# Optimization experiments

Measured on AMD Instinct MI355X. Metric: run time of the kernel, lower is better.

Reference implementation:

```python
import jax, jax.numpy as jnp
import numpy as np

EMB_DIM = 768
NUM_HEADS = 12
HEAD_DIM = EMB_DIM // NUM_HEADS
B, S = 8, 1024


def setup_inputs() -> dict:
    key = jax.random.key(0)
    ks = jax.random.split(key, 8)
    q = jax.random.normal(ks[0], (B, S, EMB_DIM), dtype=jnp.float32)
    k = jax.random.normal(ks[1], (B, S, EMB_DIM), dtype=jnp.float32)
    v = jax.random.normal(ks[2], (B, S, EMB_DIM), dtype=jnp.float32)
    # Per-head projection weights, torch nn.Linear layout [out_dim, in_dim]
    xav = float(np.sqrt(6.0 / (HEAD_DIM + HEAD_DIM)))
    Wq = jax.random.uniform(ks[3], (NUM_HEADS, HEAD_DIM, HEAD_DIM), jnp.float32, -xav, xav)
    Wk = jax.random.uniform(ks[4], (NUM_HEADS, HEAD_DIM, HEAD_DIM), jnp.float32, -xav, xav)
    Wv = jax.random.uniform(ks[5], (NUM_HEADS, HEAD_DIM, HEAD_DIM), jnp.float32, -xav, xav)
    # Output projection (torch Linear default init scale not critical for correctness baseline)
    bound = float(1.0 / np.sqrt(EMB_DIM))
    Wo = jax.random.uniform(ks[6], (EMB_DIM, EMB_DIM), jnp.float32, -bound, bound)
    bo = jax.random.uniform(ks[7], (EMB_DIM,), jnp.float32, -bound, bound)
    return {"q": q, "k": k, "v": v, "Wq": Wq, "Wk": Wk, "Wv": Wv, "Wo": Wo, "bo": bo}


def reference(q, k, v, Wq, Wk, Wv, Wo, bo):
    b, s, _ = q.shape
    # split heads: [B, S, E] -> [B, H, S, d]
    def split(x):
        return x.reshape(b, s, NUM_HEADS, HEAD_DIM).transpose(0, 2, 1, 3)
    qh, kh, vh = split(q), split(k), split(v)
    # per-head linear (torch: y = x @ W^T), vectorized over heads
    Q = jnp.einsum('bhsd,hod->bhso', qh, Wq)
    K = jnp.einsum('bhsd,hod->bhso', kh, Wk)
    V = jnp.einsum('bhsd,hod->bhso', vh, Wv)
    scale = 1.0 / jnp.sqrt(jnp.float32(HEAD_DIM))
    scores = jnp.einsum('bhqd,bhkd->bhqk', Q, K) * scale  # [B,H,S,S]
    weights = jax.nn.softmax(scores, axis=-1)
    attn = jnp.einsum('bhqk,bhkd->bhqd', weights, V)
    # merge heads: [B,H,S,d] -> [B,S,E]
    attn = attn.transpose(0, 2, 1, 3).reshape(b, s, EMB_DIM)
    return attn @ Wo.T + bo
```

## Files before the change

kernel.cpp:

```cpp
#include <hip/hip_runtime.h>
#include <hip/hip_bf16.h>

#define BB 8
#define SS 1024
#define EE 768
#define HH 12
#define DD 64
#define NT (BB*SS)

typedef __attribute__((ext_vector_type(8))) short bf16x8;
typedef __attribute__((ext_vector_type(4))) float f32x4;

__device__ __forceinline__ ushort f2bf(float f) {
  union { float f; unsigned u; } x; x.f = f;
  unsigned r = x.u + 0x7fffu + ((x.u >> 16) & 1u);
  return (ushort)(r >> 16);
}

__device__ __forceinline__ unsigned cvtpk(float a, float b) {
  unsigned r;
  asm("v_cvt_pk_bf16_f32 %0, %1, %2" : "=v"(r) : "v"(a), "v"(b));
  return r;
}

__device__ __forceinline__ void gl2lds(const void* g, void* l) {
  __builtin_amdgcn_global_load_lds(
      (const __attribute__((address_space(1))) unsigned int*)g,
      (__attribute__((address_space(3))) unsigned int*)l, 16, 0, 0);
}

__global__ void cvt_weights(const float* __restrict__ Wq, const float* __restrict__ Wk,
                            const float* __restrict__ Wv, const float* __restrict__ Wo,
                            ushort* __restrict__ Wqb, ushort* __restrict__ Wkb,
                            ushort* __restrict__ Wvb, ushort* __restrict__ Wob) {
  int i = blockIdx.x * blockDim.x + threadIdx.x;
  const int NW = HH*DD*DD;
  if (i < NW) { Wqb[i] = f2bf(Wq[i]); Wkb[i] = f2bf(Wk[i]); Wvb[i] = f2bf(Wv[i]); }
  if (i < EE*EE) Wob[i] = f2bf(Wo[i]);
}

__global__ __launch_bounds__(256) void proj_qkv(
    const float* __restrict__ q, const float* __restrict__ k, const float* __restrict__ v,
    const ushort* __restrict__ Wqb, const ushort* __restrict__ Wkb, const ushort* __restrict__ Wvb,
    ushort* __restrict__ Qb, ushort* __restrict__ Kb, ushort* __restrict__ Vt) {
  int bid = blockIdx.x;
  int m  = bid / (BB*HH*(SS/64));
  int r  = bid % (BB*HH*(SS/64));
  int bh = r / (SS/64);
  int st = r % (SS/64);

  const float*  x = (m==0 ? q : (m==1 ? k : v)) + ((size_t)((bh/HH)*SS + st*64))*EE + (bh%HH)*DD;
  const ushort* W = (m==0 ? Wqb : (m==1 ? Wkb : Wvb)) + (bh%HH)*DD*DD;

  int tid = threadIdx.x;
  int w = tid >> 6, l = tid & 63;
  int lr = l & 15, lg = l >> 4;

  bf16x8 a[2];
  const float* xr = x + (size_t)(w*16 + lr)*EE;
#pragma unroll
  for (int ks = 0; ks < 2; ++ks) {
    f32x4 t0 = *(const f32x4*)(xr + ks*32 + lg*8);
    f32x4 t1 = *(const f32x4*)(xr + ks*32 + lg*8 + 4);
    bf16x8 av;
#pragma unroll
    for (int j = 0; j < 4; ++j) { av[j] = (short)f2bf(t0[j]); av[4+j] = (short)f2bf(t1[j]); }
    a[ks] = av;
  }

  f32x4 acc[4] = {};
  if (m == 2) {
#pragma unroll
    for (int f = 0; f < 4; ++f) {
      bf16x8 b0 = *(const bf16x8*)(W + (f*16 + lr)*DD + lg*8);
      bf16x8 b1 = *(const bf16x8*)(W + (f*16 + lr)*DD + 32 + lg*8);
      acc[f] = __builtin_amdgcn_mfma_f32_16x16x32_bf16(a[0], b0, acc[f], 0, 0, 0);
      acc[f] = __builtin_amdgcn_mfma_f32_16x16x32_bf16(a[1], b1, acc[f], 0, 0, 0);
    }
    int posb = st*64 + 32*(w>>1) + 8*lg + 4*(w&1);
#pragma unroll
    for (int f = 0; f < 4; ++f) {
      ushort2 p0, p1;
      *(unsigned*)&p0 = cvtpk(acc[f][0], acc[f][1]);
      *(unsigned*)&p1 = cvtpk(acc[f][2], acc[f][3]);
      ushort4 pk; pk.x = p0.x; pk.y = p0.y; pk.z = p1.x; pk.w = p1.y;
      *(ushort4*)(Vt + ((size_t)bh*DD + f*16 + lr)*SS + posb) = pk;
    }
  } else {
#pragma unroll
    for (int f = 0; f < 4; ++f) {
      bf16x8 b0 = *(const bf16x8*)(W + (f*16 + lr)*DD + lg*8);
      bf16x8 b1 = *(const bf16x8*)(W + (f*16 + lr)*DD + 32 + lg*8);
      acc[f] = __builtin_amdgcn_mfma_f32_16x16x32_bf16(b0, a[0], acc[f], 0, 0, 0);
      acc[f] = __builtin_amdgcn_mfma_f32_16x16x32_bf16(b1, a[1], acc[f], 0, 0, 0);
    }
    float qscale = (m == 0) ? 0.18033688011112042f : 1.0f;
    ushort* dst = (m == 0 ? Qb : Kb) + ((size_t)bh*SS + st*64 + w*16 + lr)*DD;
#pragma unroll
    for (int f = 0; f < 4; ++f) {
      ushort2 p0, p1;
      *(unsigned*)&p0 = cvtpk(acc[f][0]*qscale, acc[f][1]*qscale);
      *(unsigned*)&p1 = cvtpk(acc[f][2]*qscale, acc[f][3]*qscale);
      ushort4 pk; pk.x = p0.x; pk.y = p0.y; pk.z = p1.x; pk.w = p1.y;
      *(ushort4*)(dst + f*16 + lg*4) = pk;
    }
  }
}

__global__ __launch_bounds__(256) void attn_fwd(
    const ushort* __restrict__ Qb, const ushort* __restrict__ Kb,
    const ushort* __restrict__ Vt, ushort* __restrict__ attn) {
  __shared__ uint4 ldsq[3072];
  char* ldsb = (char*)ldsq;

  int bid = blockIdx.x;
  int bh = bid % (BB*HH);
  int qt = bid / (BB*HH);
  int b = bh / HH, h = bh % HH;
  int tid = threadIdx.x, w = tid >> 6, l = tid & 63;
  int lr = l & 15, lg = l >> 4;

  const ushort* Qp0 = Qb + ((size_t)bh*SS + qt*128 + w*32 + lr)*DD;
  bf16x8 bq[2][2];
  bq[0][0] = *(const bf16x8*)(Qp0 + lg*8);
  bq[0][1] = *(const bf16x8*)(Qp0 + 32 + lg*8);
  bq[1][0] = *(const bf16x8*)(Qp0 + 16*DD + lg*8);
  bq[1][1] = *(const bf16x8*)(Qp0 + 16*DD + 32 + lg*8);

  const ushort* Kbh = Kb + (size_t)bh*SS*DD;
  const ushort* Vbh = Vt + (size_t)bh*DD*SS;

  const short ONE = (short)0x3F80;
  bf16x8 ones = {ONE, ONE, ONE, ONE, ONE, ONE, ONE, ONE};

  f32x4 lsum[2] = {};
  f32x4 o[2][4] = {};

#define STAGE(bufidx, kt) do {                                                   \
    char* LK_ = ldsb + (bufidx)*16384;                                           \
    const ushort* ksrc = Kbh + ((size_t)((kt)*64 + w*16 + lr))*DD + lg*8;        \
    const ushort* vsrc = Vbh + ((size_t)(w*16 + lr))*SS + (kt)*64 + lg*8;        \
    gl2lds(ksrc,      LK_ + tid*16);                                             \
    gl2lds(ksrc + 32, LK_ + 4096 + tid*16);                                      \
    gl2lds(vsrc,      LK_ + 8192 + tid*16);                                      \
    gl2lds(vsrc + 32, LK_ + 12288 + tid*16);                                     \
  } while (0)

  STAGE(0, 0);
  STAGE(1, 1);
  int bi = 0;
  for (int kt = 0; kt < 16; ++kt) {
    const char* LK_ = ldsb + bi*16384;
    const char* LV_ = LK_ + 8192;

    if (kt < 15) { asm volatile("s_waitcnt vmcnt(4)" ::: "memory"); }
    else         { asm volatile("s_waitcnt vmcnt(0)" ::: "memory"); }
    __builtin_amdgcn_s_barrier();
    __builtin_amdgcn_sched_barrier(0);

    int pi = bi + 2; if (pi >= 3) pi -= 3;
    if (kt < 14) STAGE(pi, kt + 2);

    f32x4 st0[4] = {}, st1[4] = {};
    __builtin_amdgcn_s_setprio(1);
#pragma unroll
    for (int f = 0; f < 4; ++f) {
      bf16x8 k0 = *(const bf16x8*)(LK_ + f*1024 + l*16);
      bf16x8 k1 = *(const bf16x8*)(LK_ + 4096 + f*1024 + l*16);
      st0[f] = __builtin_amdgcn_mfma_f32_16x16x32_bf16(k0, bq[0][0], st0[f], 0, 0, 0);
      st0[f] = __builtin_amdgcn_mfma_f32_16x16x32_bf16(k1, bq[0][1], st0[f], 0, 0, 0);
      st1[f] = __builtin_amdgcn_mfma_f32_16x16x32_bf16(k0, bq[1][0], st1[f], 0, 0, 0);
      st1[f] = __builtin_amdgcn_mfma_f32_16x16x32_bf16(k1, bq[1][1], st1[f], 0, 0, 0);
    }
    __builtin_amdgcn_s_setprio(0);

    union { bf16x8 v; unsigned u[4]; } pba[2], pbb[2];
#pragma unroll
    for (int s = 0; s < 2; ++s) {
      f32x4* st = (s == 0) ? st0 : st1;
#pragma unroll
      for (int f = 0; f < 4; ++f) {
#pragma unroll
        for (int j = 0; j < 4; ++j) st[f][j] = __builtin_amdgcn_exp2f(st[f][j]);
      }
      pba[s].u[0] = cvtpk(st[0][0], st[0][1]); pba[s].u[1] = cvtpk(st[0][2], st[0][3]);
      pba[s].u[2] = cvtpk(st[1][0], st[1][1]); pba[s].u[3] = cvtpk(st[1][2], st[1][3]);
      pbb[s].u[0] = cvtpk(st[2][0], st[2][1]); pbb[s].u[1] = cvtpk(st[2][2], st[2][3]);
      pbb[s].u[2] = cvtpk(st[3][0], st[3][1]); pbb[s].u[3] = cvtpk(st[3][2], st[3][3]);
    }

    __builtin_amdgcn_s_setprio(1);
#pragma unroll
    for (int f = 0; f < 4; ++f) {
      bf16x8 va = *(const bf16x8*)(LV_ + f*1024 + l*16);
      bf16x8 vc = *(const bf16x8*)(LV_ + 4096 + f*1024 + l*16);
      o[0][f] = __builtin_amdgcn_mfma_f32_16x16x32_bf16(va, pba[0].v, o[0][f], 0, 0, 0);
      o[0][f] = __builtin_amdgcn_mfma_f32_16x16x32_bf16(vc, pbb[0].v, o[0][f], 0, 0, 0);
      o[1][f] = __builtin_amdgcn_mfma_f32_16x16x32_bf16(va, pba[1].v, o[1][f], 0, 0, 0);
      o[1][f] = __builtin_amdgcn_mfma_f32_16x16x32_bf16(vc, pbb[1].v, o[1][f], 0, 0, 0);
    }
    lsum[0] = __builtin_amdgcn_mfma_f32_16x16x32_bf16(ones, pba[0].v, lsum[0], 0, 0, 0);
    lsum[0] = __builtin_amdgcn_mfma_f32_16x16x32_bf16(ones, pbb[0].v, lsum[0], 0, 0, 0);
    lsum[1] = __builtin_amdgcn_mfma_f32_16x16x32_bf16(ones, pba[1].v, lsum[1], 0, 0, 0);
    lsum[1] = __builtin_amdgcn_mfma_f32_16x16x32_bf16(ones, pbb[1].v, lsum[1], 0, 0, 0);
    __builtin_amdgcn_s_setprio(0);

    bi = (bi == 2) ? 0 : bi + 1;
  }
#undef STAGE

#pragma unroll
  for (int s = 0; s < 2; ++s) {
    float inv = 1.0f / lsum[s][0];
    ushort* orow = attn + ((size_t)(b*SS + qt*128 + w*32 + s*16 + lr))*EE + h*DD;
#pragma unroll
    for (int f = 0; f < 4; ++f) {
      ushort4 pkd;
      pkd.x = f2bf(o[s][f][0] * inv);
      pkd.y = f2bf(o[s][f][1] * inv);
      pkd.z = f2bf(o[s][f][2] * inv);
      pkd.w = f2bf(o[s][f][3] * inv);
      *(ushort4*)(orow + f*16 + lg*4) = pkd;
    }
  }
}

__global__ __launch_bounds__(256) void out_proj(
    const ushort* __restrict__ attn, const ushort* __restrict__ Wob,
    const float* __restrict__ bo, float* __restrict__ out) {
  __shared__ uint4 ldsq[3072];
  char* ldsb = (char*)ldsq;

  int bid = blockIdx.x;
  int mt = bid & 127;
  int nt = bid >> 7;
  int tid = threadIdx.x, w = tid >> 6, l = tid & 63;
  int lr = l & 15, lg = l >> 4;

  int rS = tid >> 3;
  int cSw = (((tid & 7) * 16) ^ ((rS & 7) << 4)) >> 1;

  const ushort* Abase = attn + ((size_t)mt*64)*EE;
  const ushort* Bbase = Wob + ((size_t)nt*128)*EE;

#define OSTAGE(bufidx, kt) do {                                                  \
    char* LA_ = ldsb + (bufidx)*24576;                                           \
    char* LB_ = LA_ + 8192;                                                      \
    const ushort* asrc = Abase + (kt)*64 + cSw;                                  \
    const ushort* bsrc = Bbase + (kt)*64 + cSw;                                  \
    gl2lds(asrc + (size_t)rS*EE,        LA_ + tid*16);                           \
    gl2lds(asrc + (size_t)(rS+32)*EE,   LA_ + 4096 + tid*16);                    \
    gl2lds(bsrc + (size_t)rS*EE,        LB_ + tid*16);                           \
    gl2lds(bsrc + (size_t)(rS+32)*EE,   LB_ + 4096 + tid*16);                    \
    gl2lds(bsrc + (size_t)(rS+64)*EE,   LB_ + 8192 + tid*16);                    \
    gl2lds(bsrc + (size_t)(rS+96)*EE,   LB_ + 12288 + tid*16);                   \
  } while (0)

  f32x4 acc[4][2] = {};

#define OCOMPUTE(bufidx) do {                                                    \
    const char* LA_ = ldsb + (bufidx)*24576;                                     \
    const char* LB_ = LA_ + 8192;                                                \
    bf16x8 af[4][2], bf[2][2];                                                   \
    _Pragma("unroll")                                                            \
    for (int f = 0; f < 4; ++f) {                                                \
      int row = f*16 + lr; int sw = (row & 7) << 4;                              \
      af[f][0] = *(const bf16x8*)(LA_ + row*128 + ((lg*16) ^ sw));               \
      af[f][1] = *(const bf16x8*)(LA_ + row*128 + ((64 + lg*16) ^ sw));          \
    }                                                                            \
    _Pragma("unroll")                                                            \
    for (int g = 0; g < 2; ++g) {                                                \
      int row = w*32 + g*16 + lr; int sw = (row & 7) << 4;                       \
      bf[g][0] = *(const bf16x8*)(LB_ + row*128 + ((lg*16) ^ sw));               \
      bf[g][1] = *(const bf16x8*)(LB_ + row*128 + ((64 + lg*16) ^ sw));          \
    }                                                                            \
    _Pragma("unroll")                                                            \
    for (int f = 0; f < 4; ++f) {                                                \
      _Pragma("unroll")                                                          \
      for (int g = 0; g < 2; ++g) {                                              \
        acc[f][g] = __builtin_amdgcn_mfma_f32_16x16x32_bf16(af[f][0], bf[g][0], acc[f][g], 0, 0, 0); \
        acc[f][g] = __builtin_amdgcn_mfma_f32_16x16x32_bf16(af[f][1], bf[g][1], acc[f][g], 0, 0, 0); \
      }                                                                          \
    }                                                                            \
  } while (0)

  OSTAGE(0, 0);
  __syncthreads();
  for (int kt = 0; kt < EE/64; ++kt) {
    if (kt < EE/64 - 1) OSTAGE((kt + 1) & 1, kt + 1);
    OCOMPUTE(kt & 1);
    __syncthreads();
  }
#undef OSTAGE
#undef OCOMPUTE

#pragma unroll
  for (int g = 0; g < 2; ++g) {
    int col = nt*128 + w*32 + g*16 + lr;
    float bias = bo[col];
#pragma unroll
    for (int f = 0; f < 4; ++f) {
#pragma unroll
      for (int j = 0; j < 4; ++j) {
        int row = mt*64 + f*16 + lg*4 + j;
        out[(size_t)row*EE + col] = acc[f][g][j] + bias;
      }
    }
  }
}

extern "C" void kernel_launch(void* const* d_in, const int* in_sizes, int n_in,
                              void* d_out, int out_size, void* d_ws, size_t ws_size,
                              hipStream_t stream) {
  (void)in_sizes; (void)n_in; (void)out_size; (void)ws_size;
  const float* q  = (const float*)d_in[0];
  const float* k  = (const float*)d_in[1];
  const float* v  = (const float*)d_in[2];
  const float* Wq = (const float*)d_in[3];
  const float* Wk = (const float*)d_in[4];
  const float* Wv = (const float*)d_in[5];
  const float* Wo = (const float*)d_in[6];
  const float* bo = (const float*)d_in[7];
  float* out = (float*)d_out;

  char* ws = (char*)d_ws;
  const size_t SZ = (size_t)BB*HH*SS*DD*2;
  ushort* Qb   = (ushort*)(ws);
  ushort* Kb   = (ushort*)(ws + SZ);
  ushort* Vt   = (ushort*)(ws + 2*SZ);
  ushort* attn = (ushort*)(ws + 3*SZ);
  ushort* Wqb  = (ushort*)(ws + 4*SZ);
  ushort* Wkb  = (ushort*)(ws + 4*SZ +   98304);
  ushort* Wvb  = (ushort*)(ws + 4*SZ + 2*98304);
  ushort* Wob  = (ushort*)(ws + 4*SZ + 3*98304);

  cvt_weights<<<(EE*EE + 255)/256, 256, 0, stream>>>(Wq, Wk, Wv, Wo, Wqb, Wkb, Wvb, Wob);
  proj_qkv<<<3*BB*HH*(SS/64), 256, 0, stream>>>(q, k, v, Wqb, Wkb, Wvb, Qb, Kb, Vt);
  attn_fwd<<<BB*HH*(SS/128), 256, 0, stream>>>(Qb, Kb, Vt, attn);
  out_proj<<<(NT/64)*(EE/128), 256, 0, stream>>>(attn, Wob, bo, out);
}
```

Measured before the change: 90.21 us.

## Convert QKV weights in-kernel and relax out_proj barriers with partial vmcnt waits

proj_qkv now reads the fp32 per-head weights directly and converts them with packed bf16 instructions, so cvt_weights only handles Wo and the separate bf16 copies of Wq/Wk/Wv go away. The input activation conversion also switches from scalar rounding to v_cvt_pk_bf16_f32. In out_proj, the full __syncthreads after each stage is replaced by raw s_barrier plus an explicit s_waitcnt vmcnt(6), so the next stage's global-to-LDS loads can stay in flight during compute. The cost is that each projection block re-reads fp32 weights, doubling weight traffic, and the code now depends on the vmcnt count matching the number of loads issued per stage.

```diff
diff --git a/kernel.cpp b/kernel.cpp
--- a/kernel.cpp
+++ b/kernel.cpp
@@ -29,19 +29,16 @@
       (__attribute__((address_space(3))) unsigned int*)l, 16, 0, 0);
 }
 
-__global__ void cvt_weights(const float* __restrict__ Wq, const float* __restrict__ Wk,
-                            const float* __restrict__ Wv, const float* __restrict__ Wo,
-                            ushort* __restrict__ Wqb, ushort* __restrict__ Wkb,
-                            ushort* __restrict__ Wvb, ushort* __restrict__ Wob) {
+#define MFMA16(A, B, C) __builtin_amdgcn_mfma_f32_16x16x32_bf16((A), (B), (C), 0, 0, 0)
+
+__global__ void cvt_weights(const float* __restrict__ Wo, ushort* __restrict__ Wob) {
   int i = blockIdx.x * blockDim.x + threadIdx.x;
-  const int NW = HH*DD*DD;
-  if (i < NW) { Wqb[i] = f2bf(Wq[i]); Wkb[i] = f2bf(Wk[i]); Wvb[i] = f2bf(Wv[i]); }
   if (i < EE*EE) Wob[i] = f2bf(Wo[i]);
 }
 
 __global__ __launch_bounds__(256) void proj_qkv(
     const float* __restrict__ q, const float* __restrict__ k, const float* __restrict__ v,
-    const ushort* __restrict__ Wqb, const ushort* __restrict__ Wkb, const ushort* __restrict__ Wvb,
+    const float* __restrict__ Wq, const float* __restrict__ Wk, const float* __restrict__ Wv,
     ushort* __restrict__ Qb, ushort* __restrict__ Kb, ushort* __restrict__ Vt) {
   int bid = blockIdx.x;
   int m  = bid / (BB*HH*(SS/64));
@@ -49,33 +46,37 @@
   int bh = r / (SS/64);
   int st = r % (SS/64);
 
-  const float*  x = (m==0 ? q : (m==1 ? k : v)) + ((size_t)((bh/HH)*SS + st*64))*EE + (bh%HH)*DD;
-  const ushort* W = (m==0 ? Wqb : (m==1 ? Wkb : Wvb)) + (bh%HH)*DD*DD;
+  const float* x = (m==0 ? q : (m==1 ? k : v)) + ((size_t)((bh/HH)*SS + st*64))*EE + (bh%HH)*DD;
+  const float* W = (m==0 ? Wq : (m==1 ? Wk : Wv)) + (bh%HH)*DD*DD;
 
   int tid = threadIdx.x;
   int w = tid >> 6, l = tid & 63;
   int lr = l & 15, lg = l >> 4;
 
-  bf16x8 a[2];
+  union { bf16x8 v; unsigned u[4]; } a[2];
   const float* xr = x + (size_t)(w*16 + lr)*EE;
 #pragma unroll
   for (int ks = 0; ks < 2; ++ks) {
     f32x4 t0 = *(const f32x4*)(xr + ks*32 + lg*8);
     f32x4 t1 = *(const f32x4*)(xr + ks*32 + lg*8 + 4);
-    bf16x8 av;
-#pragma unroll
-    for (int j = 0; j < 4; ++j) { av[j] = (short)f2bf(t0[j]); av[4+j] = (short)f2bf(t1[j]); }
-    a[ks] = av;
+    a[ks].u[0] = cvtpk(t0[0], t0[1]); a[ks].u[1] = cvtpk(t0[2], t0[3]);
+    a[ks].u[2] = cvtpk(t1[0], t1[1]); a[ks].u[3] = cvtpk(t1[2], t1[3]);
   }
 
   f32x4 acc[4] = {};
   if (m == 2) {
 #pragma unroll
     for (int f = 0; f < 4; ++f) {
-      bf16x8 b0 = *(const bf16x8*)(W + (f*16 + lr)*DD + lg*8);
-      bf16x8 b1 = *(const bf16x8*)(W + (f*16 + lr)*DD + 32 + lg*8);
-      acc[f] = __builtin_amdgcn_mfma_f32_16x16x32_bf16(a[0], b0, acc[f], 0, 0, 0);
-      acc[f] = __builtin_amdgcn_mfma_f32_16x16x32_bf16(a[1], b1, acc[f], 0, 0, 0);
+      const float* wr = W + (f*16 + lr)*DD + lg*8;
+      union { bf16x8 v; unsigned u[4]; } b0, b1;
+      f32x4 u0 = *(const f32x4*)(wr);      f32x4 u1 = *(const f32x4*)(wr + 4);
+      f32x4 u2 = *(const f32x4*)(wr + 32); f32x4 u3 = *(const f32x4*)(wr + 36);
+      b0.u[0] = cvtpk(u0[0], u0[1]); b0.u[1] = cvtpk(u0[2], u0[3]);
+      b0.u[2] = cvtpk(u1[0], u1[1]); b0.u[3] = cvtpk(u1[2], u1[3]);
+      b1.u[0] = cvtpk(u2[0], u2[1]); b1.u[1] = cvtpk(u2[2], u2[3]);
+      b1.u[2] = cvtpk(u3[0], u3[1]); b1.u[3] = cvtpk(u3[2], u3[3]);
+      acc[f] = MFMA16(a[0].v, b0.v, acc[f]);
+      acc[f] = MFMA16(a[1].v, b1.v, acc[f]);
     }
     int posb = st*64 + 32*(w>>1) + 8*lg + 4*(w&1);
 #pragma unroll
@@ -89,10 +90,16 @@
   } else {
 #pragma unroll
     for (int f = 0; f < 4; ++f) {
-      bf16x8 b0 = *(const bf16x8*)(W + (f*16 + lr)*DD + lg*8);
-      bf16x8 b1 = *(const bf16x8*)(W + (f*16 + lr)*DD + 32 + lg*8);
-      acc[f] = __builtin_amdgcn_mfma_f32_16x16x32_bf16(b0, a[0], acc[f], 0, 0, 0);
-      acc[f] = __builtin_amdgcn_mfma_f32_16x16x32_bf16(b1, a[1], acc[f], 0, 0, 0);
+      const float* wr = W + (f*16 + lr)*DD + lg*8;
+      union { bf16x8 v; unsigned u[4]; } b0, b1;
+      f32x4 u0 = *(const f32x4*)(wr);      f32x4 u1 = *(const f32x4*)(wr + 4);
+      f32x4 u2 = *(const f32x4*)(wr + 32); f32x4 u3 = *(const f32x4*)(wr + 36);
+      b0.u[0] = cvtpk(u0[0], u0[1]); b0.u[1] = cvtpk(u0[2], u0[3]);
+      b0.u[2] = cvtpk(u1[0], u1[1]); b0.u[3] = cvtpk(u1[2], u1[3]);
+      b1.u[0] = cvtpk(u2[0], u2[1]); b1.u[1] = cvtpk(u2[2], u2[3]);
+      b1.u[2] = cvtpk(u3[0], u3[1]); b1.u[3] = cvtpk(u3[2], u3[3]);
+      acc[f] = MFMA16(b0.v, a[0].v, acc[f]);
+      acc[f] = MFMA16(b1.v, a[1].v, acc[f]);
     }
     float qscale = (m == 0) ? 0.18033688011112042f : 1.0f;
     ushort* dst = (m == 0 ? Qb : Kb) + ((size_t)bh*SS + st*64 + w*16 + lr)*DD;
@@ -167,10 +174,10 @@
     for (int f = 0; f < 4; ++f) {
       bf16x8 k0 = *(const bf16x8*)(LK_ + f*1024 + l*16);
       bf16x8 k1 = *(const bf16x8*)(LK_ + 4096 + f*1024 + l*16);
-      st0[f] = __builtin_amdgcn_mfma_f32_16x16x32_bf16(k0, bq[0][0], st0[f], 0, 0, 0);
-      st0[f] = __builtin_amdgcn_mfma_f32_16x16x32_bf16(k1, bq[0][1], st0[f], 0, 0, 0);
-      st1[f] = __builtin_amdgcn_mfma_f32_16x16x32_bf16(k0, bq[1][0], st1[f], 0, 0, 0);
-      st1[f] = __builtin_amdgcn_mfma_f32_16x16x32_bf16(k1, bq[1][1], st1[f], 0, 0, 0);
+      st0[f] = MFMA16(k0, bq[0][0], st0[f]);
+      st0[f] = MFMA16(k1, bq[0][1], st0[f]);
+      st1[f] = MFMA16(k0, bq[1][0], st1[f]);
+      st1[f] = MFMA16(k1, bq[1][1], st1[f]);
     }
     __builtin_amdgcn_s_setprio(0);
 
@@ -194,15 +201,15 @@
     for (int f = 0; f < 4; ++f) {
       bf16x8 va = *(const bf16x8*)(LV_ + f*1024 + l*16);
       bf16x8 vc = *(const bf16x8*)(LV_ + 4096 + f*1024 + l*16);
-      o[0][f] = __builtin_amdgcn_mfma_f32_16x16x32_bf16(va, pba[0].v, o[0][f], 0, 0, 0);
-      o[0][f] = __builtin_amdgcn_mfma_f32_16x16x32_bf16(vc, pbb[0].v, o[0][f], 0, 0, 0);
-      o[1][f] = __builtin_amdgcn_mfma_f32_16x16x32_bf16(va, pba[1].v, o[1][f], 0, 0, 0);
-      o[1][f] = __builtin_amdgcn_mfma_f32_16x16x32_bf16(vc, pbb[1].v, o[1][f], 0, 0, 0);
-    }
-    lsum[0] = __builtin_amdgcn_mfma_f32_16x16x32_bf16(ones, pba[0].v, lsum[0], 0, 0, 0);
-    lsum[0] = __builtin_amdgcn_mfma_f32_16x16x32_bf16(ones, pbb[0].v, lsum[0], 0, 0, 0);
-    lsum[1] = __builtin_amdgcn_mfma_f32_16x16x32_bf16(ones, pba[1].v, lsum[1], 0, 0, 0);
-    lsum[1] = __builtin_amdgcn_mfma_f32_16x16x32_bf16(ones, pbb[1].v, lsum[1], 0, 0, 0);
+      o[0][f] = MFMA16(va, pba[0].v, o[0][f]);
+      o[0][f] = MFMA16(vc, pbb[0].v, o[0][f]);
+      o[1][f] = MFMA16(va, pba[1].v, o[1][f]);
+      o[1][f] = MFMA16(vc, pbb[1].v, o[1][f]);
+    }
+    lsum[0] = MFMA16(ones, pba[0].v, lsum[0]);
+    lsum[0] = MFMA16(ones, pbb[0].v, lsum[0]);
+    lsum[1] = MFMA16(ones, pba[1].v, lsum[1]);
+    lsum[1] = MFMA16(ones, pbb[1].v, lsum[1]);
     __builtin_amdgcn_s_setprio(0);
 
     bi = (bi == 2) ? 0 : bi + 1;
@@ -278,18 +285,22 @@
     for (int f = 0; f < 4; ++f) {                                                \
       _Pragma("unroll")                                                          \
       for (int g = 0; g < 2; ++g) {                                              \
-        acc[f][g] = __builtin_amdgcn_mfma_f32_16x16x32_bf16(af[f][0], bf[g][0], acc[f][g], 0, 0, 0); \
-        acc[f][g] = __builtin_amdgcn_mfma_f32_16x16x32_bf16(af[f][1], bf[g][1], acc[f][g], 0, 0, 0); \
+        acc[f][g] = MFMA16(af[f][0], bf[g][0], acc[f][g]);                       \
+        acc[f][g] = MFMA16(af[f][1], bf[g][1], acc[f][g]);                       \
       }                                                                          \
     }                                                                            \
   } while (0)
 
   OSTAGE(0, 0);
-  __syncthreads();
   for (int kt = 0; kt < EE/64; ++kt) {
     if (kt < EE/64 - 1) OSTAGE((kt + 1) & 1, kt + 1);
+    if (kt < EE/64 - 1) { asm volatile("s_waitcnt vmcnt(6)" ::: "memory"); }
+    else                { asm volatile("s_waitcnt vmcnt(0)" ::: "memory"); }
+    __builtin_amdgcn_s_barrier();
+    __builtin_amdgcn_sched_barrier(0);
     OCOMPUTE(kt & 1);
-    __syncthreads();
+    __builtin_amdgcn_s_barrier();
+    __builtin_amdgcn_sched_barrier(0);
   }
 #undef OSTAGE
 #undef OCOMPUTE
@@ -329,13 +340,10 @@
   ushort* Kb   = (ushort*)(ws + SZ);
   ushort* Vt   = (ushort*)(ws + 2*SZ);
   ushort* attn = (ushort*)(ws + 3*SZ);
-  ushort* Wqb  = (ushort*)(ws + 4*SZ);
-  ushort* Wkb  = (ushort*)(ws + 4*SZ +   98304);
-  ushort* Wvb  = (ushort*)(ws + 4*SZ + 2*98304);
-  ushort* Wob  = (ushort*)(ws + 4*SZ + 3*98304);
-
-  cvt_weights<<<(EE*EE + 255)/256, 256, 0, stream>>>(Wq, Wk, Wv, Wo, Wqb, Wkb, Wvb, Wob);
-  proj_qkv<<<3*BB*HH*(SS/64), 256, 0, stream>>>(q, k, v, Wqb, Wkb, Wvb, Qb, Kb, Vt);
+  ushort* Wob  = (ushort*)(ws + 4*SZ);
+
+  cvt_weights<<<(EE*EE + 255)/256, 256, 0, stream>>>(Wo, Wob);
+  proj_qkv<<<3*BB*HH*(SS/64), 256, 0, stream>>>(q, k, v, Wq, Wk, Wv, Qb, Kb, Vt);
   attn_fwd<<<BB*HH*(SS/128), 256, 0, stream>>>(Qb, Kb, Vt, attn);
   out_proj<<<(NT/64)*(EE/128), 256, 0, stream>>>(attn, Wob, bo, out);
 }
```

Measured after the change: 103.9 us. 1.15x slower.
